# Kernel tuning notes

Hardware: AMD Instinct MI355X
Metric: run time of the kernel (lower is better)

The kernel has to match this reference:

```python
import jax, jax.numpy as jnp
import numpy as np

B, T, D, H = 8, 4096, 512, 64

def setup_inputs() -> dict:
    key = jax.random.key(0)
    ks = jax.random.split(key, 6)
    s = 0.02  # small init scale so exp(K), exp(wbias) stay numerically tame
    return {
        "x": jax.random.normal(ks[0], (B, T, D), dtype=jnp.float32),
        "wq": jax.random.normal(ks[1], (H, D), dtype=jnp.float32) * s,
        "bq": jnp.zeros((H,), dtype=jnp.float32),
        "wk": jax.random.normal(ks[2], (H, D), dtype=jnp.float32) * s,
        "bk": jnp.zeros((H,), dtype=jnp.float32),
        "wv": jax.random.normal(ks[3], (H, D), dtype=jnp.float32) * s,
        "bv": jnp.zeros((H,), dtype=jnp.float32),
        "wp": jax.random.normal(ks[4], (D, H), dtype=jnp.float32) * s,
        "bp": jnp.zeros((D,), dtype=jnp.float32),
        "wbias": jax.random.normal(ks[5], (T, T), dtype=jnp.float32) * s,
    }

def reference(x, wq, bq, wk, bk, wv, bv, wp, bp, wbias):
    # Q, K, V projections: [B, T, H]
    Q = jnp.einsum('btd,hd->bth', x, wq) + bq
    K = jnp.einsum('btd,hd->bth', x, wk) + bk
    V = jnp.einsum('btd,hd->bth', x, wv) + bv
    ew = jnp.exp(wbias)              # [T, T], computed once
    eK = jnp.exp(K)                  # [B, T, H]
    num = jnp.einsum('ts,bsh->bth', ew, eK * V)
    den = jnp.einsum('ts,bsh->bth', ew, eK)
    Yt = jax.nn.sigmoid(Q) * (num / den)
    # output projection back to dim: [B, T, D]
    return jnp.einsum('bth,dh->btd', Yt, wp) + bp
```

## Files before the change

kernel.cpp:

```cpp
#include <hip/hip_runtime.h>
#include <math.h>

typedef _Float16 f16;
typedef __attribute__((ext_vector_type(8))) _Float16 f16x8;
typedef __attribute__((ext_vector_type(4))) _Float16 f16x4;
typedef __attribute__((ext_vector_type(4))) float f32x4;
typedef __attribute__((ext_vector_type(16))) float f32x16;

#define MFMA16(a, b, c) __builtin_amdgcn_mfma_f32_16x16x32_f16((a), (b), (c), 0, 0, 0)
#define MFMA32(a, b, c) __builtin_amdgcn_mfma_f32_32x32x16_f16((a), (b), (c), 0, 0, 0)

__device__ __forceinline__ void gld16(const f16* g, f16* l) {
  __builtin_amdgcn_global_load_lds(
      (const __attribute__((address_space(1))) unsigned int*)g,
      (__attribute__((address_space(3))) unsigned int*)l, 16, 0, 0);
}

__device__ __forceinline__ f16x8 pack8(const float* src) {
  float4 f0 = *(const float4*)src;
  float4 f1 = *(const float4*)(src + 4);
  f16x8 v;
  v[0] = (f16)f0.x; v[1] = (f16)f0.y; v[2] = (f16)f0.z; v[3] = (f16)f0.w;
  v[4] = (f16)f1.x; v[5] = (f16)f1.y; v[6] = (f16)f1.z; v[7] = (f16)f1.w;
  return v;
}

__global__ __launch_bounds__(256) void prep_ew(const float* __restrict__ wb,
                                               f16* __restrict__ ew) {
  const size_t stride = (size_t)gridDim.x * 256;
  const size_t total = (size_t)4096 * 4096 / 4;
  for (size_t i = (size_t)blockIdx.x * 256 + threadIdx.x; i < total; i += stride) {
    float4 f = ((const float4*)wb)[i];
    f16x4 o;
    o.x = (f16)expf(f.x); o.y = (f16)expf(f.y);
    o.z = (f16)expf(f.z); o.w = (f16)expf(f.w);
    ((f16x4*)ew)[i] = o;
  }
}

__global__ __launch_bounds__(256) void prep_w(const float* __restrict__ wq,
                                              const float* __restrict__ wk,
                                              const float* __restrict__ wv,
                                              const float* __restrict__ wp,
                                              f16* __restrict__ wqkvb,
                                              f16* __restrict__ wpb) {
  int i = blockIdx.x * 256 + threadIdx.x;
  wqkvb[i] = (f16)wk[i];
  wqkvb[32768 + i] = (f16)wv[i];
  wqkvb[65536 + i] = (f16)wq[i];
  wpb[i] = (f16)wp[i];
}

__global__ __launch_bounds__(256) void k1_qkv(const float* __restrict__ x,
                                              const f16* __restrict__ wqkvb,
                                              const float* __restrict__ bq,
                                              const float* __restrict__ bk,
                                              const float* __restrict__ bv,
                                              f16* __restrict__ sigQ,
                                              f16* __restrict__ XT) {
  __shared__ alignas(16) f16 sW[192 * 64];
  __shared__ alignas(16) f16 sX[64 * 64];
  const int tid = threadIdx.x;
  const int wave = tid >> 6, lane = tid & 63;
  const int m0 = blockIdx.x * 64;
  const int l15 = lane & 15;

  f32x4 accQ[4], accK[4], accV[4];
#pragma unroll
  for (int j = 0; j < 4; ++j) {
    accQ[j] = (f32x4){0.f, 0.f, 0.f, 0.f};
    accK[j] = (f32x4){0.f, 0.f, 0.f, 0.f};
    accV[j] = (f32x4){0.f, 0.f, 0.f, 0.f};
  }

  const int sc8 = tid & 7;
  const int wr8 = (tid >> 3) & 7;
  const int wcol = (sc8 ^ wr8) * 8;

  for (int ks = 0; ks < 512; ks += 64) {
#pragma unroll
    for (int q = 0; q < 6; ++q) {
      int r = q * 32 + (tid >> 3);
      gld16(wqkvb + (size_t)r * 512 + ks + wcol, &sW[r * 64 + sc8 * 8]);
    }
#pragma unroll
    for (int u = 0; u < 2; ++u) {
      int un = tid + u * 256;
      int r = un >> 3, c8 = un & 7;
      *(f16x8*)&sX[r * 64 + ((c8 ^ (r & 7)) * 8)] =
          pack8(x + (size_t)(m0 + r) * 512 + ks + c8 * 8);
    }
    __syncthreads();
#pragma unroll
    for (int kk = 0; kk < 2; ++kk) {
      const int c = kk * 4 + (lane >> 4);
      const int rK = wave * 16 + l15;
      const int rV = 64 + rK;
      f16x8 aK = *(const f16x8*)&sW[rK * 64 + ((c ^ (rK & 7)) * 8)];
      f16x8 aV = *(const f16x8*)&sW[rV * 64 + ((c ^ (rV & 7)) * 8)];
      f16x8 aQ = *(const f16x8*)&sX[rK * 64 + ((c ^ (rK & 7)) * 8)];
#pragma unroll
      for (int j = 0; j < 4; ++j) {
        const int rX = j * 16 + l15;
        const int rWq = 128 + j * 16 + l15;
        f16x8 bx = *(const f16x8*)&sX[rX * 64 + ((c ^ (rX & 7)) * 8)];
        f16x8 bw = *(const f16x8*)&sW[rWq * 64 + ((c ^ (rWq & 7)) * 8)];
        accK[j] = MFMA16(aK, bx, accK[j]);
        accV[j] = MFMA16(aV, bx, accV[j]);
        accQ[j] = MFMA16(aQ, bw, accQ[j]);
      }
    }
    __syncthreads();
  }
  const int b = m0 >> 12, t0 = m0 & 4095;
#pragma unroll
  for (int j = 0; j < 4; ++j) {
    const int h = j * 16 + l15;
    const float bqv = bq[h];
#pragma unroll
    for (int r = 0; r < 4; ++r) {
      const int m = m0 + wave * 16 + (lane >> 4) * 4 + r;
      const float v = accQ[j][r] + bqv;
      sigQ[(size_t)m * 64 + h] = (f16)(1.f / (1.f + expf(-v)));
    }
  }
#pragma unroll
  for (int r = 0; r < 4; ++r) {
    const int h = wave * 16 + (lane >> 4) * 4 + r;
    const float bkv = bk[h], bvv = bv[h];
    const size_t rowKV = (size_t)(b * 128 + h) * 4096;
    const size_t rowK = (size_t)(b * 128 + 64 + h) * 4096;
#pragma unroll
    for (int j = 0; j < 4; ++j) {
      const int t = t0 + j * 16 + l15;
      const float ek = expf(accK[j][r] + bkv);
      const float ev = accV[j][r] + bvv;
      XT[rowKV + t] = (f16)(ek * ev);
      XT[rowK + t] = (f16)ek;
    }
  }
}

__global__ __launch_bounds__(256) void k2_big(const f16* __restrict__ A,
                                              const f16* __restrict__ Bm,
                                              const f16* __restrict__ sigQ,
                                              f16* __restrict__ Yt) {
  __shared__ alignas(16) f16 sA[2][32 * 128];
  __shared__ alignas(16) f16 sB[2][64 * 128];
  const int tid = threadIdx.x;
  const int wave = tid >> 6, lane = tid & 63;
  const int wr = wave >> 1, wc = wave & 1;
  const int bid = blockIdx.x;
  const int b = (bid >> 3) & 7;
  const int m0 = ((bid & 7) + 8 * (bid >> 6)) * 64;
  const f16* Bb = Bm + (size_t)(b * 128) * 4096;

  int aRow[2], aCol[2];
#pragma unroll
  for (int q = 0; q < 2; ++q) {
    int d = q * 256 + tid;
    int lrow = d >> 4, cc = d & 15;
    int oc = cc ^ (lrow & 15);
    aRow[q] = lrow + 32 * (oc >> 3);
    aCol[q] = (oc & 7) * 8;
  }
  int bRow[4], bCol[4];
#pragma unroll
  for (int q = 0; q < 4; ++q) {
    int d = q * 256 + tid;
    int lrow = d >> 4, cc = d & 15;
    int oc = cc ^ (lrow & 15);
    bRow[q] = lrow + 64 * (oc >> 3);
    bCol[q] = (oc & 7) * 8;
  }

  f32x16 accN, accD;
#pragma unroll
  for (int r = 0; r < 16; ++r) { accN[r] = 0.f; accD[r] = 0.f; }

#define K2_STAGE(buf, ks)                                                          \
  do {                                                                             \
    _Pragma("unroll") for (int q = 0; q < 2; ++q)                                  \
        gld16(A + (size_t)(m0 + aRow[q]) * 4096 + (ks) + aCol[q],                  \
              &sA[buf][(q * 256 + tid) * 8]);                                      \
    _Pragma("unroll") for (int q = 0; q < 4; ++q)                                  \
        gld16(Bb + (size_t)bRow[q] * 4096 + (ks) + bCol[q],                        \
              &sB[buf][(q * 256 + tid) * 8]);                                      \
  } while (0)

  K2_STAGE(0, 0);
  K2_STAGE(1, 64);
  asm volatile("s_waitcnt vmcnt(6)" ::: "memory");
  __builtin_amdgcn_sched_barrier(0);
  __builtin_amdgcn_s_barrier();

  const int l31 = lane & 31, l15 = lane & 15, lhi = lane >> 5;
  const int nk = 64;
  for (int t = 0; t < nk; ++t) {
    const int cur = t & 1;
    const f16* pA = sA[cur];
    const f16* pB = sB[cur];
    __builtin_amdgcn_s_setprio(1);
#pragma unroll
    for (int kk = 0; kk < 4; ++kk) {
      const int c = kk * 2 + lhi;
      f16x8 af = *(const f16x8*)&pA[l31 * 128 + (((wr * 8 + c) ^ l15) * 8)];
      f16x8 b0 = *(const f16x8*)&pB[(wc * 32 + l31) * 128 + ((c ^ l15) * 8)];
      f16x8 b1 = *(const f16x8*)&pB[(wc * 32 + l31) * 128 + (((8 + c) ^ l15) * 8)];
      accN = MFMA32(af, b0, accN);
      accD = MFMA32(af, b1, accD);
    }
    __builtin_amdgcn_s_setprio(0);
    asm volatile("s_waitcnt lgkmcnt(0)" ::: "memory");
    __builtin_amdgcn_sched_barrier(0);
    __builtin_amdgcn_s_barrier();
    if (t + 2 < nk) {
      K2_STAGE(cur, (t + 2) * 64);
      asm volatile("s_waitcnt vmcnt(6)" ::: "memory");
    } else {
      asm volatile("s_waitcnt vmcnt(0)" ::: "memory");
    }
    __builtin_amdgcn_sched_barrier(0);
    __builtin_amdgcn_s_barrier();
  }
#undef K2_STAGE

  const int h = wc * 32 + l31;
#pragma unroll
  for (int r = 0; r < 16; ++r) {
    const int trow = m0 + wr * 32 + (r & 3) + 8 * (r >> 2) + 4 * lhi;
    const size_t mrow = (size_t)b * 4096 + trow;
    const float sq = (float)sigQ[mrow * 64 + h];
    Yt[mrow * 64 + h] = (f16)(sq * accN[r] / accD[r]);
  }
}

__global__ __launch_bounds__(256) void k4_out(const f16* __restrict__ Yt,
                                              const f16* __restrict__ wpb,
                                              const float* __restrict__ bp,
                                              float* __restrict__ out) {
  __shared__ alignas(16) f16 sA[128 * 64];
  __shared__ alignas(16) f16 sB[128 * 64];
  const int tid = threadIdx.x;
  const int wave = tid >> 6, lane = tid & 63;
  const int m0 = blockIdx.x * 128;
  const int n0 = blockIdx.y * 128;
  const int wm = (wave >> 1) * 64;
  const int wn = (wave & 1) * 64;
  const int l15 = lane & 15;
  const int sc8 = tid & 7;
  const int scol = (sc8 ^ ((tid >> 3) & 7)) * 8;

#pragma unroll
  for (int q = 0; q < 4; ++q) {
    int r = q * 32 + (tid >> 3);
    gld16(Yt + (size_t)(m0 + r) * 64 + scol, &sA[r * 64 + sc8 * 8]);
    gld16(wpb + (size_t)(n0 + r) * 64 + scol, &sB[r * 64 + sc8 * 8]);
  }
  __syncthreads();

  f32x4 acc[4][4];
#pragma unroll
  for (int i = 0; i < 4; ++i)
#pragma unroll
    for (int j = 0; j < 4; ++j) acc[i][j] = (f32x4){0.f, 0.f, 0.f, 0.f};

#pragma unroll
  for (int kk = 0; kk < 2; ++kk) {
    const int c = kk * 4 + (lane >> 4);
    f16x8 af[4], bfr[4];
#pragma unroll
    for (int i = 0; i < 4; ++i) {
      const int r = wm + i * 16 + l15;
      af[i] = *(const f16x8*)&sA[r * 64 + ((c ^ (r & 7)) * 8)];
    }
#pragma unroll
    for (int j = 0; j < 4; ++j) {
      const int r = wn + j * 16 + l15;
      bfr[j] = *(const f16x8*)&sB[r * 64 + ((c ^ (r & 7)) * 8)];
    }
#pragma unroll
    for (int i = 0; i < 4; ++i)
#pragma unroll
      for (int j = 0; j < 4; ++j) acc[i][j] = MFMA16(af[i], bfr[j], acc[i][j]);
  }

#pragma unroll
  for (int i = 0; i < 4; ++i) {
    const int row = m0 + wm + i * 16 + (lane >> 4) * 4;
#pragma unroll
    for (int j = 0; j < 4; ++j) {
      const int col = n0 + wn + j * 16 + l15;
      const float bpv = bp[col];
#pragma unroll
      for (int r = 0; r < 4; ++r)
        out[(size_t)(row + r) * 512 + col] = acc[i][j][r] + bpv;
    }
  }
}

extern "C" void kernel_launch(void* const* d_in, const int* in_sizes, int n_in,
                              void* d_out, int out_size, void* d_ws, size_t ws_size,
                              hipStream_t stream) {
  const float* x = (const float*)d_in[0];
  const float* wq = (const float*)d_in[1];
  const float* bq = (const float*)d_in[2];
  const float* wk = (const float*)d_in[3];
  const float* bk = (const float*)d_in[4];
  const float* wv = (const float*)d_in[5];
  const float* bv = (const float*)d_in[6];
  const float* wp = (const float*)d_in[7];
  const float* bp = (const float*)d_in[8];
  const float* wbias = (const float*)d_in[9];
  float* out = (float*)d_out;

  char* ws = (char*)d_ws;
  f16* ew = (f16*)(ws);
  f16* XT = (f16*)(ws + 33554432);
  f16* sigQ = (f16*)(ws + 41943040);
  f16* Yt = (f16*)(ws + 46137344);
  f16* wqkvb = (f16*)(ws + 50331648);
  f16* wpb = (f16*)(ws + 50528256);

  prep_ew<<<4096, 256, 0, stream>>>(wbias, ew);
  prep_w<<<128, 256, 0, stream>>>(wq, wk, wv, wp, wqkvb, wpb);
  k1_qkv<<<512, 256, 0, stream>>>(x, wqkvb, bq, bk, bv, sigQ, XT);
  k2_big<<<512, 256, 0, stream>>>(ew, XT, sigQ, Yt);
  k4_out<<<dim3(256, 4), 256, 0, stream>>>(Yt, wpb, bp, out);
}
```

Measured before the change: 105.7 us.

## Enlarge k2 tile to 128 rows, load B to registers, triple-buffer A

The main k2 GEMM block now covers 128 output rows using 512 threads instead of 64 rows with 256 threads, so each B (ek·v / ek) tile is reused across twice as many rows. B fragments are loaded straight from global memory into double-buffered registers rather than staged through LDS. The A tile uses a three-slot LDS ring, which cuts the loop to one barrier per k-step. The trade-offs are higher register pressure, a grid of only 256 blocks, and B loads that are less coalesced than before.

```diff
diff --git a/kernel.cpp b/kernel.cpp
--- a/kernel.cpp
+++ b/kernel.cpp
@@ -141,89 +141,111 @@
   }
 }
 
-__global__ __launch_bounds__(256) void k2_big(const f16* __restrict__ A,
+__global__ __launch_bounds__(512) void k2_big(const f16* __restrict__ A,
                                               const f16* __restrict__ Bm,
                                               const f16* __restrict__ sigQ,
                                               f16* __restrict__ Yt) {
-  __shared__ alignas(16) f16 sA[2][32 * 128];
-  __shared__ alignas(16) f16 sB[2][64 * 128];
+  __shared__ alignas(16) f16 sA[3 * 8192];
   const int tid = threadIdx.x;
   const int wave = tid >> 6, lane = tid & 63;
-  const int wr = wave >> 1, wc = wave & 1;
+  const int wr = wave >> 1;
+  const int wc = wave & 1;
   const int bid = blockIdx.x;
   const int b = (bid >> 3) & 7;
-  const int m0 = ((bid & 7) + 8 * (bid >> 6)) * 64;
-  const f16* Bb = Bm + (size_t)(b * 128) * 4096;
+  const int m0 = ((bid & 7) + 8 * (bid >> 6)) * 128;
+
+  const int l31 = lane & 31, l15 = lane & 15, lhi = lane >> 5;
 
   int aRow[2], aCol[2];
 #pragma unroll
   for (int q = 0; q < 2; ++q) {
-    int d = q * 256 + tid;
+    int d = q * 512 + tid;
     int lrow = d >> 4, cc = d & 15;
     int oc = cc ^ (lrow & 15);
-    aRow[q] = lrow + 32 * (oc >> 3);
+    aRow[q] = lrow + 64 * (oc >> 3);
     aCol[q] = (oc & 7) * 8;
   }
-  int bRow[4], bCol[4];
-#pragma unroll
-  for (int q = 0; q < 4; ++q) {
-    int d = q * 256 + tid;
-    int lrow = d >> 4, cc = d & 15;
-    int oc = cc ^ (lrow & 15);
-    bRow[q] = lrow + 64 * (oc >> 3);
-    bCol[q] = (oc & 7) * 8;
-  }
+
+  const f16* bp0 = Bm + ((size_t)(b * 128 + wc * 32 + l31)) * 4096 + lhi * 8;
+  const f16* bp1 = bp0 + (size_t)64 * 4096;
+
+  const int arow128 = ((wr & 1) * 32 + l31) * 128;
+  const int wrh8 = (wr >> 1) * 8;
 
   f32x16 accN, accD;
 #pragma unroll
   for (int r = 0; r < 16; ++r) { accN[r] = 0.f; accD[r] = 0.f; }
 
-#define K2_STAGE(buf, ks)                                                          \
-  do {                                                                             \
-    _Pragma("unroll") for (int q = 0; q < 2; ++q)                                  \
-        gld16(A + (size_t)(m0 + aRow[q]) * 4096 + (ks) + aCol[q],                  \
-              &sA[buf][(q * 256 + tid) * 8]);                                      \
-    _Pragma("unroll") for (int q = 0; q < 4; ++q)                                  \
-        gld16(Bb + (size_t)bRow[q] * 4096 + (ks) + bCol[q],                        \
-              &sB[buf][(q * 256 + tid) * 8]);                                      \
+  f16x8 bcur[8], bnxt[8];
+
+#define K2_STAGEA(off, ks)                                                      \
+  do {                                                                          \
+    _Pragma("unroll") for (int q = 0; q < 2; ++q)                               \
+        gld16(A + (size_t)(m0 + aRow[q]) * 4096 + (ks) + aCol[q],               \
+              &sA[(off) + (q * 512 + tid) * 8]);                                \
   } while (0)
 
-  K2_STAGE(0, 0);
-  K2_STAGE(1, 64);
-  asm volatile("s_waitcnt vmcnt(6)" ::: "memory");
+#define K2_LOADB(dst, T)                                                        \
+  do {                                                                          \
+    const f16* p0 = bp0 + (size_t)(T) * 64;                                     \
+    const f16* p1 = bp1 + (size_t)(T) * 64;                                     \
+    _Pragma("unroll") for (int kk = 0; kk < 4; ++kk) {                          \
+      dst[2 * kk] = *(const f16x8*)(p0 + kk * 16);                              \
+      dst[2 * kk + 1] = *(const f16x8*)(p1 + kk * 16);                          \
+    }                                                                           \
+  } while (0)
+
+#define K2_COMPUTE(bin)                                                         \
+  do {                                                                          \
+    const f16* pA = &sA[bufoff];                                                \
+    __builtin_amdgcn_s_setprio(1);                                              \
+    _Pragma("unroll") for (int kk = 0; kk < 4; ++kk) {                          \
+      const int c = kk * 2 + lhi;                                               \
+      f16x8 af = *(const f16x8*)&pA[arow128 + (((wrh8 + c) ^ l15) * 8)];        \
+      accN = MFMA32(af, bin[2 * kk], accN);                                     \
+      accD = MFMA32(af, bin[2 * kk + 1], accD);                                 \
+    }                                                                           \
+    __builtin_amdgcn_s_setprio(0);                                              \
+    bufoff += 8192; if (bufoff == 24576) bufoff = 0;                            \
+    stageoff += 8192; if (stageoff == 24576) stageoff = 0;                      \
+  } while (0)
+
+#define K2_BODY_FULL(T, bin, bout)                                              \
+  do {                                                                          \
+    K2_LOADB(bout, (T) + 1);                                                    \
+    asm volatile("s_waitcnt vmcnt(8)" ::: "memory");                            \
+    __builtin_amdgcn_sched_barrier(0);                                          \
+    __builtin_amdgcn_s_barrier();                                               \
+    __builtin_amdgcn_sched_barrier(0);                                          \
+    K2_STAGEA(stageoff, ((T) + 2) * 64);                                        \
+    K2_COMPUTE(bin);                                                            \
+  } while (0)
+
+  K2_STAGEA(0, 0);
+  K2_STAGEA(8192, 64);
+  K2_LOADB(bcur, 0);
+  int bufoff = 0, stageoff = 16384;
+
+  const int nk = 64;
+  for (int t = 0; t < nk - 2; t += 2) {
+    K2_BODY_FULL(t, bcur, bnxt);
+    K2_BODY_FULL(t + 1, bnxt, bcur);
+  }
+  K2_LOADB(bnxt, 63);
+  asm volatile("s_waitcnt vmcnt(8)" ::: "memory");
   __builtin_amdgcn_sched_barrier(0);
   __builtin_amdgcn_s_barrier();
-
-  const int l31 = lane & 31, l15 = lane & 15, lhi = lane >> 5;
-  const int nk = 64;
-  for (int t = 0; t < nk; ++t) {
-    const int cur = t & 1;
-    const f16* pA = sA[cur];
-    const f16* pB = sB[cur];
-    __builtin_amdgcn_s_setprio(1);
-#pragma unroll
-    for (int kk = 0; kk < 4; ++kk) {
-      const int c = kk * 2 + lhi;
-      f16x8 af = *(const f16x8*)&pA[l31 * 128 + (((wr * 8 + c) ^ l15) * 8)];
-      f16x8 b0 = *(const f16x8*)&pB[(wc * 32 + l31) * 128 + ((c ^ l15) * 8)];
-      f16x8 b1 = *(const f16x8*)&pB[(wc * 32 + l31) * 128 + (((8 + c) ^ l15) * 8)];
-      accN = MFMA32(af, b0, accN);
-      accD = MFMA32(af, b1, accD);
-    }
-    __builtin_amdgcn_s_setprio(0);
-    asm volatile("s_waitcnt lgkmcnt(0)" ::: "memory");
-    __builtin_amdgcn_sched_barrier(0);
-    __builtin_amdgcn_s_barrier();
-    if (t + 2 < nk) {
-      K2_STAGE(cur, (t + 2) * 64);
-      asm volatile("s_waitcnt vmcnt(6)" ::: "memory");
-    } else {
-      asm volatile("s_waitcnt vmcnt(0)" ::: "memory");
-    }
-    __builtin_amdgcn_sched_barrier(0);
-    __builtin_amdgcn_s_barrier();
-  }
-#undef K2_STAGE
+  __builtin_amdgcn_sched_barrier(0);
+  K2_COMPUTE(bcur);
+  asm volatile("s_waitcnt vmcnt(0)" ::: "memory");
+  __builtin_amdgcn_sched_barrier(0);
+  __builtin_amdgcn_s_barrier();
+  __builtin_amdgcn_sched_barrier(0);
+  K2_COMPUTE(bnxt);
+#undef K2_BODY_FULL
+#undef K2_COMPUTE
+#undef K2_LOADB
+#undef K2_STAGEA
 
   const int h = wc * 32 + l31;
 #pragma unroll
@@ -325,6 +347,6 @@
   prep_ew<<<4096, 256, 0, stream>>>(wbias, ew);
   prep_w<<<128, 256, 0, stream>>>(wq, wk, wv, wp, wqkvb, wpb);
   k1_qkv<<<512, 256, 0, stream>>>(x, wqkvb, bq, bk, bv, sigQ, XT);
-  k2_big<<<512, 256, 0, stream>>>(ew, XT, sigQ, Yt);
+  k2_big<<<256, 512, 0, stream>>>(ew, XT, sigQ, Yt);
   k4_out<<<dim3(256, 4), 256, 0, stream>>>(Yt, wpb, bp, out);
 }
```

New measurement: 192.7 us. +82.3%, slower.

## Fuse output projection into big kernel, retile with 512 threads and triple buffering

Applied to the files above, without the earlier changes.

The weight-conversion kernel is merged into the exp(wbias) prep kernel, which removes one launch. The main ew×XT GEMM is retiled to 128-row blocks with 8 waves and 16x16 MFMAs. It now uses a three-stage LDS ring with split-phase loads. The Yt normalisation and the output projection with wp are fused into its epilogue through LDS, which removes the Yt round trip to global memory and the separate k4 launch. In exchange the grid shrinks to 256 blocks, which may underfill the GPU, and the block needs 96KB of LDS.

```diff
diff --git a/kernel.cpp b/kernel.cpp
--- a/kernel.cpp
+++ b/kernel.cpp
@@ -25,8 +25,14 @@
   return v;
 }
 
-__global__ __launch_bounds__(256) void prep_ew(const float* __restrict__ wb,
-                                               f16* __restrict__ ew) {
+__global__ __launch_bounds__(256) void prep_ewpw(const float* __restrict__ wb,
+                                                 f16* __restrict__ ew,
+                                                 const float* __restrict__ wq,
+                                                 const float* __restrict__ wk,
+                                                 const float* __restrict__ wv,
+                                                 const float* __restrict__ wp,
+                                                 f16* __restrict__ wqkvb,
+                                                 f16* __restrict__ wpb) {
   const size_t stride = (size_t)gridDim.x * 256;
   const size_t total = (size_t)4096 * 4096 / 4;
   for (size_t i = (size_t)blockIdx.x * 256 + threadIdx.x; i < total; i += stride) {
@@ -36,19 +42,13 @@
     o.z = (f16)expf(f.z); o.w = (f16)expf(f.w);
     ((f16x4*)ew)[i] = o;
   }
-}
-
-__global__ __launch_bounds__(256) void prep_w(const float* __restrict__ wq,
-                                              const float* __restrict__ wk,
-                                              const float* __restrict__ wv,
-                                              const float* __restrict__ wp,
-                                              f16* __restrict__ wqkvb,
-                                              f16* __restrict__ wpb) {
-  int i = blockIdx.x * 256 + threadIdx.x;
-  wqkvb[i] = (f16)wk[i];
-  wqkvb[32768 + i] = (f16)wv[i];
-  wqkvb[65536 + i] = (f16)wq[i];
-  wpb[i] = (f16)wp[i];
+  if (blockIdx.x < 128) {
+    int i = blockIdx.x * 256 + threadIdx.x;
+    wqkvb[i] = (f16)wk[i];
+    wqkvb[32768 + i] = (f16)wv[i];
+    wqkvb[65536 + i] = (f16)wq[i];
+    wpb[i] = (f16)wp[i];
+  }
 }
 
 __global__ __launch_bounds__(256) void k1_qkv(const float* __restrict__ x,
@@ -141,162 +141,163 @@
   }
 }
 
-__global__ __launch_bounds__(256) void k2_big(const f16* __restrict__ A,
+__global__ __launch_bounds__(512) void k2_big(const f16* __restrict__ A,
                                               const f16* __restrict__ Bm,
                                               const f16* __restrict__ sigQ,
-                                              f16* __restrict__ Yt) {
-  __shared__ alignas(16) f16 sA[2][32 * 128];
-  __shared__ alignas(16) f16 sB[2][64 * 128];
-  const int tid = threadIdx.x;
-  const int wave = tid >> 6, lane = tid & 63;
-  const int wr = wave >> 1, wc = wave & 1;
-  const int bid = blockIdx.x;
-  const int b = (bid >> 3) & 7;
-  const int m0 = ((bid & 7) + 8 * (bid >> 6)) * 64;
-  const f16* Bb = Bm + (size_t)(b * 128) * 4096;
-
-  int aRow[2], aCol[2];
-#pragma unroll
-  for (int q = 0; q < 2; ++q) {
-    int d = q * 256 + tid;
-    int lrow = d >> 4, cc = d & 15;
-    int oc = cc ^ (lrow & 15);
-    aRow[q] = lrow + 32 * (oc >> 3);
-    aCol[q] = (oc & 7) * 8;
-  }
-  int bRow[4], bCol[4];
-#pragma unroll
-  for (int q = 0; q < 4; ++q) {
-    int d = q * 256 + tid;
-    int lrow = d >> 4, cc = d & 15;
-    int oc = cc ^ (lrow & 15);
-    bRow[q] = lrow + 64 * (oc >> 3);
-    bCol[q] = (oc & 7) * 8;
-  }
-
-  f32x16 accN, accD;
-#pragma unroll
-  for (int r = 0; r < 16; ++r) { accN[r] = 0.f; accD[r] = 0.f; }
-
-#define K2_STAGE(buf, ks)                                                          \
-  do {                                                                             \
-    _Pragma("unroll") for (int q = 0; q < 2; ++q)                                  \
-        gld16(A + (size_t)(m0 + aRow[q]) * 4096 + (ks) + aCol[q],                  \
-              &sA[buf][(q * 256 + tid) * 8]);                                      \
-    _Pragma("unroll") for (int q = 0; q < 4; ++q)                                  \
-        gld16(Bb + (size_t)bRow[q] * 4096 + (ks) + bCol[q],                        \
-              &sB[buf][(q * 256 + tid) * 8]);                                      \
-  } while (0)
-
-  K2_STAGE(0, 0);
-  K2_STAGE(1, 64);
-  asm volatile("s_waitcnt vmcnt(6)" ::: "memory");
-  __builtin_amdgcn_sched_barrier(0);
-  __builtin_amdgcn_s_barrier();
-
-  const int l31 = lane & 31, l15 = lane & 15, lhi = lane >> 5;
-  const int nk = 64;
-  for (int t = 0; t < nk; ++t) {
-    const int cur = t & 1;
-    const f16* pA = sA[cur];
-    const f16* pB = sB[cur];
-    __builtin_amdgcn_s_setprio(1);
-#pragma unroll
-    for (int kk = 0; kk < 4; ++kk) {
-      const int c = kk * 2 + lhi;
-      f16x8 af = *(const f16x8*)&pA[l31 * 128 + (((wr * 8 + c) ^ l15) * 8)];
-      f16x8 b0 = *(const f16x8*)&pB[(wc * 32 + l31) * 128 + ((c ^ l15) * 8)];
-      f16x8 b1 = *(const f16x8*)&pB[(wc * 32 + l31) * 128 + (((8 + c) ^ l15) * 8)];
-      accN = MFMA32(af, b0, accN);
-      accD = MFMA32(af, b1, accD);
-    }
-    __builtin_amdgcn_s_setprio(0);
-    asm volatile("s_waitcnt lgkmcnt(0)" ::: "memory");
-    __builtin_amdgcn_sched_barrier(0);
-    __builtin_amdgcn_s_barrier();
-    if (t + 2 < nk) {
-      K2_STAGE(cur, (t + 2) * 64);
-      asm volatile("s_waitcnt vmcnt(6)" ::: "memory");
-    } else {
-      asm volatile("s_waitcnt vmcnt(0)" ::: "memory");
-    }
-    __builtin_amdgcn_sched_barrier(0);
-    __builtin_amdgcn_s_barrier();
-  }
-#undef K2_STAGE
-
-  const int h = wc * 32 + l31;
-#pragma unroll
-  for (int r = 0; r < 16; ++r) {
-    const int trow = m0 + wr * 32 + (r & 3) + 8 * (r >> 2) + 4 * lhi;
-    const size_t mrow = (size_t)b * 4096 + trow;
-    const float sq = (float)sigQ[mrow * 64 + h];
-    Yt[mrow * 64 + h] = (f16)(sq * accN[r] / accD[r]);
-  }
-}
-
-__global__ __launch_bounds__(256) void k4_out(const f16* __restrict__ Yt,
                                               const f16* __restrict__ wpb,
                                               const float* __restrict__ bp,
                                               float* __restrict__ out) {
-  __shared__ alignas(16) f16 sA[128 * 64];
-  __shared__ alignas(16) f16 sB[128 * 64];
+  __shared__ alignas(16) f16 smem[3 * 16384];
   const int tid = threadIdx.x;
-  const int wave = tid >> 6, lane = tid & 63;
-  const int m0 = blockIdx.x * 128;
-  const int n0 = blockIdx.y * 128;
-  const int wm = (wave >> 1) * 64;
-  const int wn = (wave & 1) * 64;
-  const int l15 = lane & 15;
-  const int sc8 = tid & 7;
-  const int scol = (sc8 ^ ((tid >> 3) & 7)) * 8;
-
-#pragma unroll
-  for (int q = 0; q < 4; ++q) {
-    int r = q * 32 + (tid >> 3);
-    gld16(Yt + (size_t)(m0 + r) * 64 + scol, &sA[r * 64 + sc8 * 8]);
-    gld16(wpb + (size_t)(n0 + r) * 64 + scol, &sB[r * 64 + sc8 * 8]);
-  }
+  const int w = tid >> 6, lane = tid & 63;
+  const int wm6 = w >> 2;
+  const int wn = w & 3;
+  const int bid = blockIdx.x;
+  const int b = (bid >> 3) & 7;
+  const int m0 = ((bid & 7) + 8 * (bid >> 6)) * 128;
+  const f16* Bb = Bm + (size_t)(b * 128) * 4096;
+
+  const int l31 = lane & 31, l15 = lane & 15, lhi = lane >> 5;
+  const int hi4 = (lane >> 4) & 3;
+
+  int sRow[2], sCol[2];
+#pragma unroll
+  for (int u = 0; u < 2; ++u) {
+    int d = u * 512 + tid;
+    int lrow = d >> 4, cc = d & 15;
+    int oc = cc ^ (lrow & 15);
+    sRow[u] = lrow + 64 * (oc >> 3);
+    sCol[u] = (oc & 7) * 8;
+  }
+
+  f32x4 accN[4], accD[4];
+#pragma unroll
+  for (int i = 0; i < 4; ++i) {
+    accN[i] = (f32x4){0.f, 0.f, 0.f, 0.f};
+    accD[i] = (f32x4){0.f, 0.f, 0.f, 0.f};
+  }
+
+#define SB0 __builtin_amdgcn_sched_barrier(0)
+#define K2_STAGE_U(bb, ks, u)                                                  \
+  do {                                                                         \
+    gld16(A + (size_t)(m0 + sRow[u]) * 4096 + (ks) + sCol[u],                  \
+          &smem[(bb) + ((u) * 512 + tid) * 8]);                                \
+    gld16(Bb + (size_t)sRow[u] * 4096 + (ks) + sCol[u],                        \
+          &smem[(bb) + 8192 + ((u) * 512 + tid) * 8]);                         \
+  } while (0)
+
+  const int am8 = wm6 * 8;
+  const int bprow = (wn * 16 + l15) * 128;
+
+#define K2_PHASE(bb, kh, bb2, ks2, DOSTAGE, VMC)                               \
+  do {                                                                         \
+    const f16* pA = &smem[bb];                                                 \
+    const f16* pB = &smem[(bb) + 8192];                                        \
+    const int c = (kh) * 4 + hi4;                                              \
+    f16x8 af0 = *(const f16x8*)&pA[(0 * 16 + l15) * 128 + (((c + am8) ^ l15) * 8)]; \
+    f16x8 af1 = *(const f16x8*)&pA[(1 * 16 + l15) * 128 + (((c + am8) ^ l15) * 8)]; \
+    f16x8 af2 = *(const f16x8*)&pA[(2 * 16 + l15) * 128 + (((c + am8) ^ l15) * 8)]; \
+    f16x8 af3 = *(const f16x8*)&pA[(3 * 16 + l15) * 128 + (((c + am8) ^ l15) * 8)]; \
+    f16x8 bn = *(const f16x8*)&pB[bprow + ((c ^ l15) * 8)];                    \
+    f16x8 bd = *(const f16x8*)&pB[bprow + (((c + 8) ^ l15) * 8)];              \
+    if (DOSTAGE) K2_STAGE_U(bb2, ks2, kh);                                     \
+    SB0;                                                                       \
+    __builtin_amdgcn_s_barrier();                                              \
+    SB0;                                                                       \
+    asm volatile("s_waitcnt lgkmcnt(0)" ::: "memory");                         \
+    SB0;                                                                       \
+    __builtin_amdgcn_s_setprio(1);                                             \
+    accN[0] = MFMA16(af0, bn, accN[0]); accD[0] = MFMA16(af0, bd, accD[0]);    \
+    accN[1] = MFMA16(af1, bn, accN[1]); accD[1] = MFMA16(af1, bd, accD[1]);    \
+    accN[2] = MFMA16(af2, bn, accN[2]); accD[2] = MFMA16(af2, bd, accD[2]);    \
+    accN[3] = MFMA16(af3, bn, accN[3]); accD[3] = MFMA16(af3, bd, accD[3]);    \
+    __builtin_amdgcn_s_setprio(0);                                             \
+    if ((VMC) == 4) asm volatile("s_waitcnt vmcnt(4)" ::: "memory");           \
+    if ((VMC) == 0) asm volatile("s_waitcnt vmcnt(0)" ::: "memory");           \
+    SB0;                                                                       \
+    __builtin_amdgcn_s_barrier();                                              \
+    SB0;                                                                       \
+  } while (0)
+
+  K2_STAGE_U(0, 0, 0);
+  K2_STAGE_U(0, 0, 1);
+  K2_STAGE_U(16384, 64, 0);
+  K2_STAGE_U(16384, 64, 1);
+  asm volatile("s_waitcnt vmcnt(4)" ::: "memory");
+  SB0;
+  __builtin_amdgcn_s_barrier();
+  SB0;
+
+  const int nk = 64;
+  int bo = 0;
+  for (int t = 0; t < nk - 2; ++t) {
+    int bb2 = bo + 32768;
+    if (bb2 >= 49152) bb2 -= 49152;
+    const int ks2 = (t + 2) * 64;
+    K2_PHASE(bo, 0, bb2, ks2, 1, -1);
+    K2_PHASE(bo, 1, bb2, ks2, 1, 4);
+    bo += 16384;
+    if (bo == 49152) bo = 0;
+  }
+  K2_PHASE(bo, 0, 0, 0, 0, -1);
+  K2_PHASE(bo, 1, 0, 0, 0, 0);
+  bo += 16384;
+  if (bo == 49152) bo = 0;
+  K2_PHASE(bo, 0, 0, 0, 0, -1);
+  K2_PHASE(bo, 1, 0, 0, 0, -1);
+#undef K2_PHASE
+#undef K2_STAGE_U
+
   __syncthreads();
-
-  f32x4 acc[4][4];
-#pragma unroll
-  for (int i = 0; i < 4; ++i)
-#pragma unroll
-    for (int j = 0; j < 4; ++j) acc[i][j] = (f32x4){0.f, 0.f, 0.f, 0.f};
-
-#pragma unroll
-  for (int kk = 0; kk < 2; ++kk) {
-    const int c = kk * 4 + (lane >> 4);
-    f16x8 af[4], bfr[4];
-#pragma unroll
-    for (int i = 0; i < 4; ++i) {
-      const int r = wm + i * 16 + l15;
-      af[i] = *(const f16x8*)&sA[r * 64 + ((c ^ (r & 7)) * 8)];
-    }
-#pragma unroll
-    for (int j = 0; j < 4; ++j) {
-      const int r = wn + j * 16 + l15;
-      bfr[j] = *(const f16x8*)&sB[r * 64 + ((c ^ (r & 7)) * 8)];
-    }
-#pragma unroll
-    for (int i = 0; i < 4; ++i)
-#pragma unroll
-      for (int j = 0; j < 4; ++j) acc[i][j] = MFMA16(af[i], bfr[j], acc[i][j]);
-  }
-
+  f16* sYt = smem;
+  f16* sWp = smem + 8704;
+  const int wm = wm6 * 64;
 #pragma unroll
   for (int i = 0; i < 4; ++i) {
-    const int row = m0 + wm + i * 16 + (lane >> 4) * 4;
-#pragma unroll
-    for (int j = 0; j < 4; ++j) {
-      const int col = n0 + wn + j * 16 + l15;
-      const float bpv = bp[col];
-#pragma unroll
-      for (int r = 0; r < 4; ++r)
-        out[(size_t)(row + r) * 512 + col] = acc[i][j][r] + bpv;
-    }
-  }
+#pragma unroll
+    for (int r = 0; r < 4; ++r) {
+      const int tr = wm + i * 16 + (lane >> 4) * 4 + r;
+      const int h = wn * 16 + l15;
+      const size_t mrow = (size_t)b * 4096 + m0 + tr;
+      const float sq = (float)sigQ[mrow * 64 + h];
+      sYt[tr * 68 + h] = (f16)(sq * accN[i][r] / accD[i][r]);
+    }
+  }
+#pragma unroll
+  for (int u = 0; u < 8; ++u) {
+    const int d = u * 512 + tid;
+    f16x8 v = *(const f16x8*)(wpb + (size_t)d * 8);
+    *(f16x8*)&sWp[(d >> 3) * 68 + (d & 7) * 8] = v;
+  }
+  __syncthreads();
+
+  f32x16 oacc[8];
+#pragma unroll
+  for (int cb = 0; cb < 8; ++cb)
+#pragma unroll
+    for (int r = 0; r < 16; ++r) oacc[cb][r] = 0.f;
+  const int yr = (w & 3) * 32 + l31;
+  const int dbase = (w >> 2) * 256;
+#pragma unroll
+  for (int c = 0; c < 4; ++c) {
+    f16x8 ay = *(const f16x8*)&sYt[yr * 68 + c * 16 + lhi * 8];
+#pragma unroll
+    for (int cb = 0; cb < 8; ++cb) {
+      f16x8 bw = *(const f16x8*)&sWp[(dbase + cb * 32 + l31) * 68 + c * 16 + lhi * 8];
+      oacc[cb] = MFMA32(ay, bw, oacc[cb]);
+    }
+  }
+#pragma unroll
+  for (int cb = 0; cb < 8; ++cb) {
+    const int od = dbase + cb * 32 + l31;
+    const float bpv = bp[od];
+#pragma unroll
+    for (int r = 0; r < 16; ++r) {
+      const int orow = (w & 3) * 32 + (r & 3) + 8 * (r >> 2) + 4 * lhi;
+      out[((size_t)(b * 4096 + m0 + orow)) * 512 + od] = oacc[cb][r] + bpv;
+    }
+  }
+#undef SB0
 }
 
 extern "C" void kernel_launch(void* const* d_in, const int* in_sizes, int n_in,
@@ -318,13 +319,10 @@
   f16* ew = (f16*)(ws);
   f16* XT = (f16*)(ws + 33554432);
   f16* sigQ = (f16*)(ws + 41943040);
-  f16* Yt = (f16*)(ws + 46137344);
-  f16* wqkvb = (f16*)(ws + 50331648);
-  f16* wpb = (f16*)(ws + 50528256);
-
-  prep_ew<<<4096, 256, 0, stream>>>(wbias, ew);
-  prep_w<<<128, 256, 0, stream>>>(wq, wk, wv, wp, wqkvb, wpb);
+  f16* wqkvb = (f16*)(ws + 46137344);
+  f16* wpb = (f16*)(ws + 46333952);
+
+  prep_ewpw<<<4096, 256, 0, stream>>>(wbias, ew, wq, wk, wv, wp, wqkvb, wpb);
   k1_qkv<<<512, 256, 0, stream>>>(x, wqkvb, bq, bk, bv, sigQ, XT);
-  k2_big<<<512, 256, 0, stream>>>(ew, XT, sigQ, Yt);
-  k4_out<<<dim3(256, 4), 256, 0, stream>>>(Yt, wpb, bp, out);
-}
+  k2_big<<<256, 512, 0, stream>>>(ew, XT, sigQ, wpb, bp, out);
+}
```

Result: faster. 95.52 us (-9.6%).
